# Performance work log

Measured on AMD Instinct MI355X. Metric: run time of the kernel, lower is better.

## Reference

```python
import jax, jax.numpy as jnp
import numpy as np

IN_MODES = (40, 32, 25)    # prod = 32000 = num_embeddings
OUT_MODES = (8, 8, 16)     # prod = 1024  = embedding_dim
RANKS = (1, 16, 16, 1)
B, T = 4, 4096


def setup_inputs() -> dict:
    key = jax.random.key(0)
    k0, k1, k2, kid = jax.random.split(key, 4)
    # cores G_k: (r_k, out_k, in_k, r_{k+1}); xavier-ish scale
    def core(k, rk, om, im, rk1):
        fan = rk + om * im * rk1
        scale = jnp.sqrt(6.0 / fan)
        return jax.random.uniform(k, (rk, om, im, rk1), jnp.float32, -scale, scale)
    core0 = core(k0, RANKS[0], OUT_MODES[0], IN_MODES[0], RANKS[1])
    core1 = core(k1, RANKS[1], OUT_MODES[1], IN_MODES[1], RANKS[2])
    core2 = core(k2, RANKS[2], OUT_MODES[2], IN_MODES[2], RANKS[3])
    input_ids = jax.random.randint(kid, (B, T), 0, int(np.prod(IN_MODES)), dtype=jnp.int64)
    return {"core0": core0, "core1": core1, "core2": core2, "input_ids": input_ids}


def reference(core0, core1, core2, input_ids):
    V = int(np.prod(IN_MODES))
    E = int(np.prod(OUT_MODES))
    # TT reconstruction: contract over ranks a,b,c,d (a=d=1),
    # out modes x,y,z first, then in modes p,q,r (matches torch eq order)
    T_full = jnp.einsum('axpb,byqc,czrd->xyzpqr', core0, core1, core2)
    W = T_full.reshape(E, V).T  # (num_embeddings, embedding_dim)
    return W[input_ids]  # (B, T, E)
```

## Files before the change

kernel.cpp:

```cpp
#include <hip/hip_runtime.h>
#include <hip/hip_bf16.h>


#define T12_FLOATS (40 * 32 * 16 * 64)
#define C2T_FLOATS (25 * 16 * 16)

typedef float v4f __attribute__((ext_vector_type(4)));

__global__ __launch_bounds__(256) void tt_precompute_kernel(
    const float* __restrict__ core0, const float* __restrict__ core1,
    const float* __restrict__ core2, float* __restrict__ T12,
    float* __restrict__ C2T) {
  if (blockIdx.x == 1280) {
    for (int i = threadIdx.x; i < C2T_FLOATS; i += 256) {
      int r = i >> 8;
      int cz = i & 255;
      C2T[i] = core2[cz * 25 + r];
    }
    return;
  }
  int pq = blockIdx.x;
  int p = pq >> 5;
  int q = pq & 31;

  __shared__ float sA[8 * 16];
  __shared__ float sB[16 * 8 * 16];

  for (int i = threadIdx.x; i < 128; i += 256) {
    int x = i >> 4, b = i & 15;
    sA[i] = core0[(x * 40 + p) * 16 + b];
  }
  for (int i = threadIdx.x; i < 2048; i += 256) {
    int b = i >> 7;
    int yc = i & 127;
    int y = yc >> 4, c = yc & 15;
    sB[i] = core1[((b * 8 + y) * 32 + q) * 16 + c];
  }
  __syncthreads();

  float* dst = T12 + pq * 1024;
  int xy = threadIdx.x & 63;
  int x = xy >> 3, y = xy & 7;
  for (int c = threadIdx.x >> 6; c < 16; c += 4) {
    float acc = 0.f;
#pragma unroll
    for (int b = 0; b < 16; b++) acc += sA[x * 16 + b] * sB[b * 128 + y * 16 + c];
    dst[c * 64 + xy] = acc;
  }
}

__global__ __launch_bounds__(256) void tt_gather_kernel(
    const float* __restrict__ T12, const float* __restrict__ C2T,
    const int* __restrict__ ids, float* __restrict__ out) {
  int wave = threadIdx.x >> 6;
  int lane = threadIdx.x & 63;
  int xyg = lane >> 2;
  int zg = lane & 3;
  int tbase = blockIdx.x * 4 + wave;

  for (int k = 0; k < 2; k++) {
    int t = tbase + k * 8192;

    int id = ids[t];
    int p = id / 800;
    int rem = id - p * 800;
    int q = rem / 25;
    int r = rem - q * 25;

    const v4f* E = (const v4f*)(T12 + (p * 32 + q) * 1024);
    const v4f* C = (const v4f*)(C2T + r * 256);

    float acc[4][4];
#pragma unroll
    for (int i = 0; i < 4; i++)
#pragma unroll
      for (int j = 0; j < 4; j++) acc[i][j] = 0.f;

#pragma unroll
    for (int c = 0; c < 16; c++) {
      v4f e4 = E[c * 16 + xyg];
      v4f w4 = C[c * 4 + zg];
#pragma unroll
      for (int i = 0; i < 4; i++)
#pragma unroll
        for (int j = 0; j < 4; j++) acc[i][j] += e4[i] * w4[j];
    }

    float* dst = out + (size_t)t * 1024 + xyg * 64 + zg * 4;
#pragma unroll
    for (int i = 0; i < 4; i++) {
      v4f v = {acc[i][0], acc[i][1], acc[i][2], acc[i][3]};
      __builtin_nontemporal_store(v, (v4f*)(dst + i * 16));
    }
  }
}

extern "C" void kernel_launch(void* const* d_in, const int* in_sizes, int n_in,
                              void* d_out, int out_size, void* d_ws, size_t ws_size,
                              hipStream_t stream) {
  const float* core0 = (const float*)d_in[0];
  const float* core1 = (const float*)d_in[1];
  const float* core2 = (const float*)d_in[2];
  const int* ids = (const int*)d_in[3];
  float* out = (float*)d_out;

  float* T12 = (float*)d_ws;
  float* C2T = T12 + T12_FLOATS;

  tt_precompute_kernel<<<dim3(1281), dim3(256), 0, stream>>>(core0, core1, core2, T12, C2T);
  tt_gather_kernel<<<dim3(2048), dim3(256), 0, stream>>>(T12, C2T, ids, out);
}
```

Measured before the change: 102.8 us.

## Fuse TT precompute into gather kernel, computing per-token core0×core1 slice on the fly

Drops the separate precompute kernel and the 5 MB T12 workspace. Each wave now builds its token's 16x64 core0·core1 slice in shared memory straight from the cores, with core2 transposed into shared memory once per block. The goal is to remove a kernel launch and the global write and re-read of T12, paid for with redundant per-token contraction work and extra block-wide syncs. The output write of about 67 MB likely still dominates.

Result: slower. 117.4 us (+14.2%).

```diff
diff --git a/kernel.cpp b/kernel.cpp
--- a/kernel.cpp
+++ b/kernel.cpp
@@ -2,96 +2,83 @@
 #include <hip/hip_bf16.h>
 
 
-#define T12_FLOATS (40 * 32 * 16 * 64)
-#define C2T_FLOATS (25 * 16 * 16)
-
 typedef float v4f __attribute__((ext_vector_type(4)));
 
-__global__ __launch_bounds__(256) void tt_precompute_kernel(
+__global__ __launch_bounds__(512) void tt_fused_kernel(
     const float* __restrict__ core0, const float* __restrict__ core1,
-    const float* __restrict__ core2, float* __restrict__ T12,
-    float* __restrict__ C2T) {
-  if (blockIdx.x == 1280) {
-    for (int i = threadIdx.x; i < C2T_FLOATS; i += 256) {
-      int r = i >> 8;
-      int cz = i & 255;
-      C2T[i] = core2[cz * 25 + r];
-    }
-    return;
-  }
-  int pq = blockIdx.x;
-  int p = pq >> 5;
-  int q = pq & 31;
+    const float* __restrict__ core2, const int* __restrict__ ids,
+    float* __restrict__ out) {
+  __shared__ __align__(16) float sC2T[25 * 256];
+  __shared__ __align__(16) float sE[8 * 1088];
 
-  __shared__ float sA[8 * 16];
-  __shared__ float sB[16 * 8 * 16];
-
-  for (int i = threadIdx.x; i < 128; i += 256) {
-    int x = i >> 4, b = i & 15;
-    sA[i] = core0[(x * 40 + p) * 16 + b];
-  }
-  for (int i = threadIdx.x; i < 2048; i += 256) {
-    int b = i >> 7;
-    int yc = i & 127;
-    int y = yc >> 4, c = yc & 15;
-    sB[i] = core1[((b * 8 + y) * 32 + q) * 16 + c];
+  for (int i = threadIdx.x; i < 6400; i += 512) {
+    int r = i >> 8, cz = i & 255;
+    sC2T[i] = core2[cz * 25 + r];
   }
   __syncthreads();
 
-  float* dst = T12 + pq * 1024;
-  int xy = threadIdx.x & 63;
-  int x = xy >> 3, y = xy & 7;
-  for (int c = threadIdx.x >> 6; c < 16; c += 4) {
-    float acc = 0.f;
+  const int wave = threadIdx.x >> 6;
+  const int lane = threadIdx.x & 63;
+  float* __restrict__ Ew = sE + wave * 1088;
+
+  const int ey = lane & 7;
+  const int ec0 = lane >> 3;
+  const int xyg = lane >> 2;
+  const int zg = lane & 3;
+
+  const int tbase = (blockIdx.x * 8 + wave) * 2;
+
+  for (int k = 0; k < 2; ++k) {
+    const int t = tbase + k;
+    int id = ids[t];
+    int p = __builtin_amdgcn_readfirstlane(id / 800);
+    int rem = id - p * 800;
+    int q = __builtin_amdgcn_readfirstlane(rem / 25);
+    int r = __builtin_amdgcn_readfirstlane(rem - q * 25);
+
+    const float* __restrict__ A0 = core0 + p * 16;
+    const float* __restrict__ B1 = core1 + q * 16 + ey * 512 + ec0;
+
 #pragma unroll
-    for (int b = 0; b < 16; b++) acc += sA[x * 16 + b] * sB[b * 128 + y * 16 + c];
-    dst[c * 64 + xy] = acc;
-  }
-}
-
-__global__ __launch_bounds__(256) void tt_gather_kernel(
-    const float* __restrict__ T12, const float* __restrict__ C2T,
-    const int* __restrict__ ids, float* __restrict__ out) {
-  int wave = threadIdx.x >> 6;
-  int lane = threadIdx.x & 63;
-  int xyg = lane >> 2;
-  int zg = lane & 3;
-  int tbase = blockIdx.x * 4 + wave;
-
-  for (int k = 0; k < 2; k++) {
-    int t = tbase + k * 8192;
-
-    int id = ids[t];
-    int p = id / 800;
-    int rem = id - p * 800;
-    int q = rem / 25;
-    int r = rem - q * 25;
-
-    const v4f* E = (const v4f*)(T12 + (p * 32 + q) * 1024);
-    const v4f* C = (const v4f*)(C2T + r * 256);
+    for (int pp = 0; pp < 2; ++pp) {
+      float bcol[16];
+#pragma unroll
+      for (int b = 0; b < 16; ++b) bcol[b] = B1[b * 4096 + pp * 8];
+      const int c = ec0 + pp * 8;
+#pragma unroll
+      for (int x = 0; x < 8; ++x) {
+        float acc = 0.f;
+#pragma unroll
+        for (int b = 0; b < 16; ++b) acc += A0[x * 640 + b] * bcol[b];
+        Ew[c * 68 + x * 8 + ey] = acc;
+      }
+    }
+    __syncthreads();
 
     float acc[4][4];
 #pragma unroll
-    for (int i = 0; i < 4; i++)
+    for (int i = 0; i < 4; ++i)
 #pragma unroll
-      for (int j = 0; j < 4; j++) acc[i][j] = 0.f;
+      for (int j = 0; j < 4; ++j) acc[i][j] = 0.f;
 
+    const float* Cr = sC2T + r * 256;
 #pragma unroll
-    for (int c = 0; c < 16; c++) {
-      v4f e4 = E[c * 16 + xyg];
-      v4f w4 = C[c * 4 + zg];
+    for (int c = 0; c < 16; ++c) {
+      v4f e4 = *(const v4f*)(Ew + c * 68 + xyg * 4);
+      v4f c4 = *(const v4f*)(Cr + c * 16 + zg * 4);
 #pragma unroll
-      for (int i = 0; i < 4; i++)
+      for (int i = 0; i < 4; ++i)
 #pragma unroll
-        for (int j = 0; j < 4; j++) acc[i][j] += e4[i] * w4[j];
+        for (int j = 0; j < 4; ++j) acc[i][j] += e4[i] * c4[j];
     }
 
     float* dst = out + (size_t)t * 1024 + xyg * 64 + zg * 4;
 #pragma unroll
-    for (int i = 0; i < 4; i++) {
+    for (int i = 0; i < 4; ++i) {
       v4f v = {acc[i][0], acc[i][1], acc[i][2], acc[i][3]};
       __builtin_nontemporal_store(v, (v4f*)(dst + i * 16));
     }
+    __syncthreads();
   }
 }
 
@@ -104,9 +91,5 @@
   const int* ids = (const int*)d_in[3];
   float* out = (float*)d_out;
 
-  float* T12 = (float*)d_ws;
-  float* C2T = T12 + T12_FLOATS;
-
-  tt_precompute_kernel<<<dim3(1281), dim3(256), 0, stream>>>(core0, core1, core2, T12, C2T);
-  tt_gather_kernel<<<dim3(2048), dim3(256), 0, stream>>>(T12, C2T, ids, out);
+  tt_fused_kernel<<<dim3(1024), dim3(512), 0, stream>>>(core0, core1, core2, ids, out);
 }
```
